# Optimization experiments

Measured on AMD Instinct MI355X. Metric: run time of the kernel, lower is better.

The kernel has to match this reference:

```python
import jax, jax.numpy as jnp
import numpy as np

B, S, HID = 2, 8192, 1024
NH, DH, CL = 16, 64, 128
NB, NA = 1, 0  # num_chunks_before, num_chunks_after
NC = S // CL
MASK_VALUE = -1e9


def _look_adjacent(v):
    # v: [..., n_chunks, chunk_len(*d)] with chunk axis=2; torch's
    # cat([v[:,:,i:], v[:,:,:i]], dim=2) == jnp.roll(v, -i, axis=2)
    slices = [jnp.roll(v, -i, axis=2) for i in range(-NB, NA + 1)]
    return jnp.concatenate(slices, axis=3)


def setup_inputs() -> dict:
    key = jax.random.key(0)
    k1, k2, k3, k4 = jax.random.split(key, 4)
    scale = 1.0 / np.sqrt(HID).astype(np.float32)
    hidden_states = jax.random.normal(k1, (B, S, HID), jnp.float32)
    Wq = jax.random.normal(k2, (HID, NH * DH), jnp.float32) * scale
    Wk = jax.random.normal(k3, (HID, NH * DH), jnp.float32) * scale
    Wv = jax.random.normal(k4, (HID, NH * DH), jnp.float32) * scale
    return {"hidden_states": hidden_states, "Wq": Wq, "Wk": Wk, "Wv": Wv}


def _forward(hidden_states, Wq, Wk, Wv):
    # project and split heads -> [B, NH, NC, CL, DH]
    def proj(W):
        x = (hidden_states @ W).reshape(B, S, NH, DH)
        return x.transpose(0, 2, 1, 3).reshape(B, NH, NC, CL, DH)

    q = proj(Wq)
    k = proj(Wk) / jnp.sqrt(jnp.asarray(DH, hidden_states.dtype))
    v = proj(Wv)

    k_adj = _look_adjacent(k)  # [B, NH, NC, (NB+1+NA)*CL, DH]
    v_adj = _look_adjacent(v)

    # per-chunk scores: [B, NH, NC, CL, (NB+1+NA)*CL]
    dots = jnp.einsum("bhnqd,bhnkd->bhnqk", q, k_adj)

    # causal mask via position indices (decoder). Chunk 0's wrapped-around
    # keys carry large indices and are correctly masked out.
    idx = jnp.arange(S).reshape(1, 1, NC, CL)
    kv_idx = _look_adjacent(idx)  # [1, 1, NC, (NB+1+NA)*CL]
    causal = idx[..., :, None] >= kv_idx[..., None, :]
    dots = jnp.where(causal, dots, jnp.asarray(MASK_VALUE, dots.dtype))

    probs = jax.nn.softmax(dots, axis=-1)
    out = jnp.einsum("bhnqk,bhnkd->bhnqd", probs, v_adj)
    # merge chunks and heads -> [B, S, NH*DH]
    out = out.reshape(B, NH, S, DH).transpose(0, 2, 1, 3).reshape(B, S, NH * DH)
    return out


def reference(hidden_states, Wq, Wk, Wv):
    return _forward(hidden_states, Wq, Wk, Wv)
```

## Files before the change

### kernel.cpp

```cpp
#include <hip/hip_runtime.h>
#include <stdint.h>


typedef unsigned short u16;
typedef __bf16 bf16x8 __attribute__((ext_vector_type(8)));
typedef float f32x4 __attribute__((ext_vector_type(4)));

typedef __attribute__((address_space(1))) void* gas_ptr;
typedef __attribute__((address_space(3))) void* las_ptr;

__device__ __forceinline__ u16 f2bf(float f) {
  uint32_t u = __float_as_uint(f);
  u += 0x7fffu + ((u >> 16) & 1u);
  return (u16)(u >> 16);
}

__device__ __forceinline__ void gload16(const void* g, void* l) {
  __builtin_amdgcn_global_load_lds((gas_ptr)g, (las_ptr)l, 16, 0, 0);
}

__global__ void k_conv_x(const float* __restrict__ x, u16* __restrict__ o, int n4) {
  int i = blockIdx.x * blockDim.x + threadIdx.x;
  int stride = gridDim.x * blockDim.x;
  for (; i < n4; i += stride) {
    float4 v = reinterpret_cast<const float4*>(x)[i];
    unsigned long long pk = (unsigned long long)f2bf(v.x) |
                            ((unsigned long long)f2bf(v.y) << 16) |
                            ((unsigned long long)f2bf(v.z) << 32) |
                            ((unsigned long long)f2bf(v.w) << 48);
    reinterpret_cast<unsigned long long*>(o)[i] = pk;
  }
}

__global__ void k_conv_w(const float* __restrict__ wq, const float* __restrict__ wk,
                         const float* __restrict__ wv, u16* __restrict__ wt) {
  __shared__ float tile[32][33];
  int z = blockIdx.z;
  const float* src = (z == 0) ? wq : (z == 1) ? wk : wv;
  float scale = (z == 1) ? 0.125f : 1.0f;
  int n0 = blockIdx.x * 32, k0 = blockIdx.y * 32;
  int tx = threadIdx.x, ty = threadIdx.y;
  for (int i = ty; i < 32; i += 8)
    tile[i][tx] = src[(size_t)(k0 + i) * 1024 + n0 + tx];
  __syncthreads();
  u16* dst = wt + (size_t)z * 1024 * 1024;
  for (int i = ty; i < 32; i += 8)
    dst[(size_t)(n0 + i) * 1024 + k0 + tx] = f2bf(tile[tx][i] * scale);
}

__global__ __launch_bounds__(512, 2) void k_gemmf(const u16* __restrict__ xb,
                                                  const u16* __restrict__ wt,
                                                  u16* __restrict__ q_ws,
                                                  u16* __restrict__ k_ws,
                                                  u16* __restrict__ v_t) {
  __shared__ __align__(16) char lds[131072];
  char* As = lds;
  char* Bs = lds + 65536;
  const int tid = threadIdx.x;
  const int lane = tid & 63, l16 = lane & 15, lhi = lane >> 4;
  const int wave = tid >> 6;
  const int wm = (wave >> 2) * 128;
  const int wn = (wave & 3) * 64;

  const int bid = blockIdx.x;
  const int wg = (bid & 7) * 96 + (bid >> 3);
  const int mp = wg / 12;
  const int np = wg % 12;
  const int z = np >> 2;
  const int m0 = mp * 256;
  const int n0 = (np & 3) * 256;
  const u16* wz = wt + (size_t)z * 1024 * 1024;

  const int lrow8 = lane >> 3;
  const int scolx = ((lane & 7) * 16) ^ (lrow8 << 4);

  const int j0 = wave * 2, j1 = wave * 2 + 1;
  const int rbA00 = 8 * j0 + 64 * (0 + (j0 >> 3)), rbA01 = 8 * j1 + 64 * (0 + (j1 >> 3));
  const int rbA10 = 8 * j0 + 64 * (1 + (j0 >> 3)), rbA11 = 8 * j1 + 64 * (1 + (j1 >> 3));
  const int rbB00 = 8 * (j0 & 3) + (j0 >> 2) * 64, rbB01 = 8 * (j1 & 3) + (j1 >> 2) * 64;
  const int rbB10 = rbB00 + 32, rbB11 = rbB01 + 32;
  const char* aB = (const char*)xb + (size_t)m0 * 2048 + scolx;
  const char* bB = (const char*)wz + (size_t)n0 * 2048 + scolx;

  f32x4 acc[8][4] = {};

  auto stageAll = [&](int buf, int kt) {
    const size_t ko = (size_t)kt * 128;
    char* Ad = As + buf * 32768;
    char* Bd = Bs + buf * 32768;
    gload16(aB + (size_t)(rbA00 + lrow8) * 2048 + ko, Ad + rbA00 * 128);
    gload16(aB + (size_t)(rbA01 + lrow8) * 2048 + ko, Ad + rbA01 * 128);
    gload16(aB + (size_t)(rbA10 + lrow8) * 2048 + ko, Ad + rbA10 * 128);
    gload16(aB + (size_t)(rbA11 + lrow8) * 2048 + ko, Ad + rbA11 * 128);
    gload16(bB + (size_t)(rbB00 + lrow8) * 2048 + ko, Bd + rbB00 * 128);
    gload16(bB + (size_t)(rbB01 + lrow8) * 2048 + ko, Bd + rbB01 * 128);
    gload16(bB + (size_t)(rbB10 + lrow8) * 2048 + ko, Bd + rbB10 * 128);
    gload16(bB + (size_t)(rbB11 + lrow8) * 2048 + ko, Bd + rbB11 * 128);
  };

  stageAll(0, 0);

  const bool swapped = (z < 2);

  for (int t = 0; t < 16; ++t) {
    const int cbuf = t & 1, nbuf = cbuf ^ 1;
    const int ktn = (t < 15) ? t + 1 : 15;
    __syncthreads();
    stageAll(nbuf, ktn);
#pragma unroll
    for (int mh = 0; mh < 2; ++mh) {
      bf16x8 af[4][2];
#pragma unroll
      for (int fi = 0; fi < 4; ++fi) {
        int row = wm + (mh * 4 + fi) * 16 + l16;
#pragma unroll
        for (int ks = 0; ks < 2; ++ks)
          af[fi][ks] = *(const bf16x8*)(As + cbuf * 32768 + row * 128 +
                                        ((ks * 64 + lhi * 16) ^ ((row & 7) << 4)));
      }
#pragma unroll
      for (int nh = 0; nh < 2; ++nh) {
        bf16x8 bfr[2][2];
#pragma unroll
        for (int f2 = 0; f2 < 2; ++f2) {
          int rn = wn + nh * 32 + f2 * 16 + l16;
#pragma unroll
          for (int ks = 0; ks < 2; ++ks)
            bfr[f2][ks] = *(const bf16x8*)(Bs + cbuf * 32768 + rn * 128 +
                                           ((ks * 64 + lhi * 16) ^ ((rn & 7) << 4)));
        }
        __builtin_amdgcn_s_setprio(1);
        if (swapped) {
#pragma unroll
          for (int fi = 0; fi < 4; ++fi)
#pragma unroll
            for (int f2 = 0; f2 < 2; ++f2)
#pragma unroll
              for (int ks = 0; ks < 2; ++ks)
                acc[mh * 4 + fi][nh * 2 + f2] = __builtin_amdgcn_mfma_f32_16x16x32_bf16(
                    bfr[f2][ks], af[fi][ks], acc[mh * 4 + fi][nh * 2 + f2], 0, 0, 0);
        } else {
#pragma unroll
          for (int fi = 0; fi < 4; ++fi)
#pragma unroll
            for (int f2 = 0; f2 < 2; ++f2)
#pragma unroll
              for (int ks = 0; ks < 2; ++ks)
                acc[mh * 4 + fi][nh * 2 + f2] = __builtin_amdgcn_mfma_f32_16x16x32_bf16(
                    af[fi][ks], bfr[f2][ks], acc[mh * 4 + fi][nh * 2 + f2], 0, 0, 0);
        }
        __builtin_amdgcn_s_setprio(0);
      }
    }
  }

  if (swapped) {
    u16* o = (z == 0) ? q_ws : k_ws;
#pragma unroll
    for (int fr = 0; fr < 8; ++fr) {
#pragma unroll
      for (int fn = 0; fn < 4; ++fn) {
        int m = m0 + wm + fr * 16 + l16;
        int n = n0 + wn + fn * 16 + lhi * 4;
        unsigned long long pk = (unsigned long long)f2bf(acc[fr][fn][0]) |
                                ((unsigned long long)f2bf(acc[fr][fn][1]) << 16) |
                                ((unsigned long long)f2bf(acc[fr][fn][2]) << 32) |
                                ((unsigned long long)f2bf(acc[fr][fn][3]) << 48);
        *(unsigned long long*)((char*)o + ((size_t)m * 1024 + n) * 2) = pk;
      }
    }
  } else {
#pragma unroll
    for (int fr = 0; fr < 8; ++fr) {
#pragma unroll
      for (int fn = 0; fn < 4; ++fn) {
        int m = m0 + wm + fr * 16 + lhi * 4;
        int n = n0 + wn + fn * 16 + l16;
        int bb = m >> 13;
        int s = m & 8191;
        unsigned long long pk = (unsigned long long)f2bf(acc[fr][fn][0]) |
                                ((unsigned long long)f2bf(acc[fr][fn][1]) << 16) |
                                ((unsigned long long)f2bf(acc[fr][fn][2]) << 32) |
                                ((unsigned long long)f2bf(acc[fr][fn][3]) << 48);
        *(unsigned long long*)((char*)v_t + ((size_t)(bb * 1024 + n) * 8192 + s) * 2) = pk;
      }
    }
  }
}

__global__ __launch_bounds__(256, 2) void k_attn(const u16* __restrict__ qw,
                                                 const u16* __restrict__ kw,
                                                 const u16* __restrict__ vt,
                                                 float* __restrict__ out) {
  __shared__ __align__(16) char lds[81920];
  char* q_s = lds;
  char* k_s = lds + 16384;
  char* v_s = lds + 49152;
  const int tid = threadIdx.x;
  const int lane = tid & 63, l16 = lane & 15, lhi = lane >> 4;
  const int wave = tid >> 6;
  char* p_s = lds + wave * 8192;
  const int c = blockIdx.x & 63;
  const int h = (blockIdx.x >> 6) & 15;
  const int b = blockIdx.x >> 10;
  const int cprev = (c == 0) ? 0 : c - 1;
  const int dstb = (tid & 192) * 16;

#pragma unroll
  for (int it = 0; it < 4; ++it) {
    int idx = it * 256 + tid;
    int row = idx >> 3, colb = (idx & 7) * 16;
    gload16((const char*)qw + ((size_t)(b * 8192 + c * 128 + row) * 1024 + h * 64) * 2 +
                (colb ^ ((row & 7) << 4)),
            q_s + it * 4096 + dstb);
  }
#pragma unroll
  for (int it = 0; it < 8; ++it) {
    int idx = it * 256 + tid;
    int row = idx >> 3, colb = (idx & 7) * 16;
    int srow = (row < 128) ? (cprev * 128 + row) : (c * 128 + row - 128);
    gload16((const char*)kw + ((size_t)(b * 8192 + srow) * 1024 + h * 64) * 2 +
                (colb ^ ((row & 7) << 4)),
            k_s + it * 4096 + dstb);
  }
#pragma unroll
  for (int it = 0; it < 8; ++it) {
    int idx = it * 256 + tid;
    int row = idx >> 5;
    int colb = (idx & 31) * 16;
    int colbl = colb ^ ((row & 7) << 4);
    size_t roff = ((size_t)((b * 16 + h) * 64 + row)) * 8192 * 2;
    size_t soff = c ? ((size_t)(c * 128 - 128) * 2 + colbl) : (size_t)(colbl & 255);
    gload16((const char*)vt + roff + soff, v_s + it * 4096 + dstb);
  }
  __syncthreads();

  const int rbase = wave * 32;
  f32x4 accs[2][16];
#pragma unroll
  for (int rb = 0; rb < 2; ++rb)
#pragma unroll
    for (int nb = 0; nb < 16; ++nb) accs[rb][nb] = f32x4{0.f, 0.f, 0.f, 0.f};

#pragma unroll
  for (int ks = 0; ks < 2; ++ks) {
    bf16x8 af[2];
#pragma unroll
    for (int rb = 0; rb < 2; ++rb) {
      int row = rbase + rb * 16 + l16;
      af[rb] = *(const bf16x8*)(q_s + row * 128 + ((ks * 64 + lhi * 16) ^ ((row & 7) << 4)));
    }
#pragma unroll
    for (int nb = 0; nb < 16; ++nb) {
      int row = nb * 16 + l16;
      bf16x8 bfb = *(const bf16x8*)(k_s + row * 128 + ((ks * 64 + lhi * 16) ^ ((row & 7) << 4)));
#pragma unroll
      for (int rb = 0; rb < 2; ++rb)
        accs[rb][nb] = __builtin_amdgcn_mfma_f32_16x16x32_bf16(af[rb], bfb, accs[rb][nb], 0, 0, 0);
    }
  }

  float rinv[2][4];
#pragma unroll
  for (int rb = 0; rb < 2; ++rb) {
#pragma unroll
    for (int j = 0; j < 4; ++j) {
      int qi = rbase + rb * 16 + lhi * 4 + j;
      float m = -3.0e38f;
#pragma unroll
      for (int nb = 0; nb < 16; ++nb) {
        int kl = nb * 16 + l16;
        float v = accs[rb][nb][j];
        bool valid = (kl <= qi + 128) && ((c > 0) || (kl >= 128));
        v = valid ? v : -1.0e9f;
        accs[rb][nb][j] = v;
        m = fmaxf(m, v);
      }
#pragma unroll
      for (int d = 1; d < 16; d <<= 1) m = fmaxf(m, __shfl_xor(m, d));
      float s = 0.f;
#pragma unroll
      for (int nb = 0; nb < 16; ++nb) {
        float e = __expf(accs[rb][nb][j] - m);
        accs[rb][nb][j] = e;
        s += e;
      }
#pragma unroll
      for (int d = 1; d < 16; d <<= 1) s += __shfl_xor(s, d);
      rinv[rb][j] = 1.0f / s;
    }
  }

  __syncthreads();

  f32x4 acco[2][4] = {};
#pragma unroll
  for (int half = 0; half < 2; ++half) {
#pragma unroll
    for (int rb = 0; rb < 2; ++rb) {
#pragma unroll
      for (int nbh = 0; nbh < 8; ++nbh) {
#pragma unroll
        for (int j = 0; j < 4; ++j) {
          int r = rb * 16 + lhi * 4 + j;
          int cb = (nbh * 16 + l16) * 2;
          *(u16*)(p_s + r * 256 + (cb ^ ((r & 7) << 4))) = f2bf(accs[rb][half * 8 + nbh][j]);
        }
      }
    }
    __asm__ volatile("s_waitcnt lgkmcnt(0)" ::: "memory");
    __builtin_amdgcn_sched_barrier(0);
#pragma unroll
    for (int ks = 0; ks < 4; ++ks) {
      bf16x8 pf[2];
#pragma unroll
      for (int rb = 0; rb < 2; ++rb) {
        int r = rb * 16 + l16;
        pf[rb] = *(const bf16x8*)(p_s + r * 256 + ((ks * 64 + lhi * 16) ^ ((r & 7) << 4)));
      }
#pragma unroll
      for (int db = 0; db < 4; ++db) {
        int vr = db * 16 + l16;
        bf16x8 vf = *(const bf16x8*)(v_s + vr * 512 +
                                     ((half * 256 + ks * 64 + lhi * 16) ^ ((vr & 7) << 4)));
#pragma unroll
        for (int rb = 0; rb < 2; ++rb)
          acco[rb][db] = __builtin_amdgcn_mfma_f32_16x16x32_bf16(pf[rb], vf, acco[rb][db], 0, 0, 0);
      }
    }
    if (half == 0) {
      __asm__ volatile("s_waitcnt lgkmcnt(0)" ::: "memory");
      __builtin_amdgcn_sched_barrier(0);
    }
  }

#pragma unroll
  for (int rb = 0; rb < 2; ++rb) {
#pragma unroll
    for (int db = 0; db < 4; ++db) {
#pragma unroll
      for (int j = 0; j < 4; ++j) {
        int r = rbase + rb * 16 + lhi * 4 + j;
        out[(size_t)(b * 8192 + c * 128 + r) * 1024 + h * 64 + db * 16 + l16] =
            acco[rb][db][j] * rinv[rb][j];
      }
    }
  }
}

extern "C" void kernel_launch(void* const* d_in, const int* in_sizes, int n_in,
                              void* d_out, int out_size, void* d_ws, size_t ws_size,
                              hipStream_t stream) {
  const float* hs = (const float*)d_in[0];
  const float* wq = (const float*)d_in[1];
  const float* wk = (const float*)d_in[2];
  const float* wv = (const float*)d_in[3];
  float* out = (float*)d_out;
  char* ws = (char*)d_ws;

  u16* x_bf = (u16*)ws;
  u16* wt   = (u16*)(ws + 33554432);
  u16* q_ws = (u16*)(ws + 39845888);
  u16* k_ws = (u16*)(ws + 73400320);
  u16* v_t  = (u16*)(ws + 106954752);

  k_conv_x<<<dim3(2048), dim3(256), 0, stream>>>(hs, x_bf, 16384 * 1024 / 4);
  k_conv_w<<<dim3(32, 32, 3), dim3(32, 8), 0, stream>>>(wq, wk, wv, wt);
  k_gemmf<<<dim3(768), dim3(512), 0, stream>>>(x_bf, wt, q_ws, k_ws, v_t);
  k_attn<<<dim3(2048), dim3(256), 0, stream>>>(q_ws, k_ws, v_t, out);
}
```

Baseline: 301.9 us.

## Pipeline QKV projection GEMM with finer-grained half-tile staging and explicit waitcnts

Replaces the simple double-buffered loop, which waited on a full-tile __syncthreads, with an eight-phase-per-two-k-tiles schedule. Each phase stages one half of the A or B tile for a future k-step, and waits only on the global_load_lds groups it needs using explicit vmcnt counts. sched_barrier and s_barrier fence the phases so that LDS reads and global loads interleave with the MFMA blocks. The aim is better latency hiding in the projection GEMM, at the cost of more barriers and fragile hand-tuned waitcnt accounting.

```diff
diff --git a/kernel.cpp b/kernel.cpp
--- a/kernel.cpp
+++ b/kernel.cpp
@@ -74,85 +74,115 @@
   const int lrow8 = lane >> 3;
   const int scolx = ((lane & 7) * 16) ^ (lrow8 << 4);
 
-  const int j0 = wave * 2, j1 = wave * 2 + 1;
-  const int rbA00 = 8 * j0 + 64 * (0 + (j0 >> 3)), rbA01 = 8 * j1 + 64 * (0 + (j1 >> 3));
-  const int rbA10 = 8 * j0 + 64 * (1 + (j0 >> 3)), rbA11 = 8 * j1 + 64 * (1 + (j1 >> 3));
-  const int rbB00 = 8 * (j0 & 3) + (j0 >> 2) * 64, rbB01 = 8 * (j1 & 3) + (j1 >> 2) * 64;
-  const int rbB10 = rbB00 + 32, rbB11 = rbB01 + 32;
   const char* aB = (const char*)xb + (size_t)m0 * 2048 + scolx;
   const char* bB = (const char*)wz + (size_t)n0 * 2048 + scolx;
 
   f32x4 acc[8][4] = {};
 
-  auto stageAll = [&](int buf, int kt) {
+  auto stageA = [&](int buf, int kt, int h) {
     const size_t ko = (size_t)kt * 128;
     char* Ad = As + buf * 32768;
+#pragma unroll
+    for (int i = 0; i < 2; ++i) {
+      int j = wave * 2 + i;
+      int rb = 8 * j + 64 * (h + (j >> 3));
+      gload16(aB + (size_t)(rb + lrow8) * 2048 + ko, Ad + rb * 128);
+    }
+  };
+  auto stageB = [&](int buf, int kt, int h) {
+    const size_t ko = (size_t)kt * 128;
     char* Bd = Bs + buf * 32768;
-    gload16(aB + (size_t)(rbA00 + lrow8) * 2048 + ko, Ad + rbA00 * 128);
-    gload16(aB + (size_t)(rbA01 + lrow8) * 2048 + ko, Ad + rbA01 * 128);
-    gload16(aB + (size_t)(rbA10 + lrow8) * 2048 + ko, Ad + rbA10 * 128);
-    gload16(aB + (size_t)(rbA11 + lrow8) * 2048 + ko, Ad + rbA11 * 128);
-    gload16(bB + (size_t)(rbB00 + lrow8) * 2048 + ko, Bd + rbB00 * 128);
-    gload16(bB + (size_t)(rbB01 + lrow8) * 2048 + ko, Bd + rbB01 * 128);
-    gload16(bB + (size_t)(rbB10 + lrow8) * 2048 + ko, Bd + rbB10 * 128);
-    gload16(bB + (size_t)(rbB11 + lrow8) * 2048 + ko, Bd + rbB11 * 128);
+#pragma unroll
+    for (int i = 0; i < 2; ++i) {
+      int j = wave * 2 + i;
+      int rb = 8 * (j & 3) + (j >> 2) * 64 + h * 32;
+      gload16(bB + (size_t)(rb + lrow8) * 2048 + ko, Bd + rb * 128);
+    }
   };
 
-  stageAll(0, 0);
-
   const bool swapped = (z < 2);
 
-  for (int t = 0; t < 16; ++t) {
-    const int cbuf = t & 1, nbuf = cbuf ^ 1;
-    const int ktn = (t < 15) ? t + 1 : 15;
-    __syncthreads();
-    stageAll(nbuf, ktn);
-#pragma unroll
-    for (int mh = 0; mh < 2; ++mh) {
-      bf16x8 af[4][2];
-#pragma unroll
-      for (int fi = 0; fi < 4; ++fi) {
-        int row = wm + (mh * 4 + fi) * 16 + l16;
-#pragma unroll
-        for (int ks = 0; ks < 2; ++ks)
-          af[fi][ks] = *(const bf16x8*)(As + cbuf * 32768 + row * 128 +
-                                        ((ks * 64 + lhi * 16) ^ ((row & 7) << 4)));
-      }
-#pragma unroll
-      for (int nh = 0; nh < 2; ++nh) {
-        bf16x8 bfr[2][2];
-#pragma unroll
-        for (int f2 = 0; f2 < 2; ++f2) {
-          int rn = wn + nh * 32 + f2 * 16 + l16;
+  auto loadA = [&](int cb, int mh, bf16x8 af[4][2]) {
+#pragma unroll
+    for (int fi = 0; fi < 4; ++fi) {
+      int row = wm + mh * 64 + fi * 16 + l16;
+#pragma unroll
+      for (int ks = 0; ks < 2; ++ks)
+        af[fi][ks] = *(const bf16x8*)(As + cb * 32768 + row * 128 +
+                                      ((ks * 64 + lhi * 16) ^ ((row & 7) << 4)));
+    }
+  };
+  auto loadB = [&](int cb, int nh, bf16x8 bfr[2][2]) {
+#pragma unroll
+    for (int f2 = 0; f2 < 2; ++f2) {
+      int rn = wn + nh * 32 + f2 * 16 + l16;
+#pragma unroll
+      for (int ks = 0; ks < 2; ++ks)
+        bfr[f2][ks] = *(const bf16x8*)(Bs + cb * 32768 + rn * 128 +
+                                       ((ks * 64 + lhi * 16) ^ ((rn & 7) << 4)));
+    }
+  };
+  auto domfma = [&](int mh, int nh, bf16x8 af[4][2], bf16x8 bfr[2][2]) {
+    if (swapped) {
+#pragma unroll
+      for (int fi = 0; fi < 4; ++fi)
+#pragma unroll
+        for (int f2 = 0; f2 < 2; ++f2)
 #pragma unroll
           for (int ks = 0; ks < 2; ++ks)
-            bfr[f2][ks] = *(const bf16x8*)(Bs + cbuf * 32768 + rn * 128 +
-                                           ((ks * 64 + lhi * 16) ^ ((rn & 7) << 4)));
-        }
-        __builtin_amdgcn_s_setprio(1);
-        if (swapped) {
-#pragma unroll
-          for (int fi = 0; fi < 4; ++fi)
-#pragma unroll
-            for (int f2 = 0; f2 < 2; ++f2)
-#pragma unroll
-              for (int ks = 0; ks < 2; ++ks)
-                acc[mh * 4 + fi][nh * 2 + f2] = __builtin_amdgcn_mfma_f32_16x16x32_bf16(
-                    bfr[f2][ks], af[fi][ks], acc[mh * 4 + fi][nh * 2 + f2], 0, 0, 0);
-        } else {
-#pragma unroll
-          for (int fi = 0; fi < 4; ++fi)
-#pragma unroll
-            for (int f2 = 0; f2 < 2; ++f2)
-#pragma unroll
-              for (int ks = 0; ks < 2; ++ks)
-                acc[mh * 4 + fi][nh * 2 + f2] = __builtin_amdgcn_mfma_f32_16x16x32_bf16(
-                    af[fi][ks], bfr[f2][ks], acc[mh * 4 + fi][nh * 2 + f2], 0, 0, 0);
-        }
-        __builtin_amdgcn_s_setprio(0);
-      }
-    }
-  }
+            acc[mh * 4 + fi][nh * 2 + f2] = __builtin_amdgcn_mfma_f32_16x16x32_bf16(
+                bfr[f2][ks], af[fi][ks], acc[mh * 4 + fi][nh * 2 + f2], 0, 0, 0);
+    } else {
+#pragma unroll
+      for (int fi = 0; fi < 4; ++fi)
+#pragma unroll
+        for (int f2 = 0; f2 < 2; ++f2)
+#pragma unroll
+          for (int ks = 0; ks < 2; ++ks)
+            acc[mh * 4 + fi][nh * 2 + f2] = __builtin_amdgcn_mfma_f32_16x16x32_bf16(
+                af[fi][ks], bfr[f2][ks], acc[mh * 4 + fi][nh * 2 + f2], 0, 0, 0);
+    }
+  };
+
+#define PHASE(CB, MH, NH, STAGE_STMT, VMN)                          \
+  do {                                                              \
+    bf16x8 af[4][2], bfr[2][2];                                     \
+    loadA(CB, MH, af);                                              \
+    loadB(CB, NH, bfr);                                             \
+    STAGE_STMT;                                                     \
+    if (VMN == 6) asm volatile("s_waitcnt vmcnt(6)" ::: "memory");  \
+    if (VMN == 8) asm volatile("s_waitcnt vmcnt(8)" ::: "memory");  \
+    __builtin_amdgcn_sched_barrier(0);                              \
+    __builtin_amdgcn_s_barrier();                                   \
+    asm volatile("s_waitcnt lgkmcnt(0)" ::: "memory");              \
+    __builtin_amdgcn_sched_barrier(0);                              \
+    __builtin_amdgcn_s_setprio(1);                                  \
+    domfma(MH, NH, af, bfr);                                        \
+    __builtin_amdgcn_s_setprio(0);                                  \
+    __builtin_amdgcn_sched_barrier(0);                              \
+    __builtin_amdgcn_s_barrier();                                   \
+  } while (0)
+
+  stageA(0, 0, 0); stageB(0, 0, 0); stageA(0, 0, 1); stageB(0, 0, 1);
+  stageA(1, 1, 0); stageB(1, 1, 0);
+  asm volatile("s_waitcnt vmcnt(8)" ::: "memory");
+  __builtin_amdgcn_sched_barrier(0);
+  __builtin_amdgcn_s_barrier();
+
+  for (int i = 0; i < 8; ++i) {
+    const int t = 2 * i;
+    const int k2 = (t + 2 < 16) ? t + 2 : 15;
+    const int k3 = (t + 3 < 16) ? t + 3 : 15;
+    PHASE(0, 0, 0, stageA(1, t + 1, 1), 6);
+    PHASE(0, 0, 1, stageB(1, t + 1, 1), -1);
+    PHASE(0, 1, 0, stageA(0, k2, 0), -1);
+    PHASE(0, 1, 1, stageB(0, k2, 0), 8);
+    PHASE(1, 0, 0, stageA(0, k2, 1), 6);
+    PHASE(1, 0, 1, stageB(0, k2, 1), -1);
+    PHASE(1, 1, 0, stageA(1, k3, 0), -1);
+    PHASE(1, 1, 1, stageB(1, k3, 0), 8);
+  }
+#undef PHASE
 
   if (swapped) {
     u16* o = (z == 0) ? q_ws : k_ws;
```

New measurement: 523.0 us. +73.3%, slower.
